# Kernel optimization log

Hardware: AMD Instinct MI355X
Metric: run time of the kernel (lower is better)

The kernel has to match this reference:

```python
import jax, jax.numpy as jnp
import numpy as np

DIM, NH, NKV = 1024, 16, 4
HD = DIM // NH  # 64
B, T = 2, 2048


def _rotary_freqs(seq_len, dim):
    inv_freq = 1.0 / (10000.0 ** (jnp.arange(0, dim, 2, dtype=jnp.float32) / dim))
    pos = jnp.arange(seq_len, dtype=jnp.float32)
    return pos[:, None] * inv_freq[None, :]  # [T, dim/2]


def _apply_rotary(x, freqs):
    # x: [B, H, T, HD]; freqs: [T, HD/2]
    x1, x2 = x[..., ::2], x[..., 1::2]
    cos, sin = jnp.cos(freqs), jnp.sin(freqs)
    # NOTE: faithful to source, second half is x1*sin - x2*cos (not +)
    return jnp.concatenate([x1 * cos - x2 * sin, x1 * sin - x2 * cos], axis=-1)


def setup_inputs() -> dict:
    key = jax.random.key(0)
    ks = jax.random.split(key, 5)
    s = 0.02
    return {
        "x": jax.random.normal(ks[0], (B, T, DIM), dtype=jnp.float32),
        "Wq": jax.random.normal(ks[1], (DIM, DIM), dtype=jnp.float32) * s,
        "bq": jnp.zeros((DIM,), jnp.float32),
        "Wk": jax.random.normal(ks[2], (DIM, NKV * HD), dtype=jnp.float32) * s,
        "bk": jnp.zeros((NKV * HD,), jnp.float32),
        "Wv": jax.random.normal(ks[3], (DIM, NKV * HD), dtype=jnp.float32) * s,
        "bv": jnp.zeros((NKV * HD,), jnp.float32),
        "Wo": jax.random.normal(ks[4], (DIM, DIM), dtype=jnp.float32) * s,
        "bo": jnp.zeros((DIM,), jnp.float32),
    }


def reference(x, Wq, bq, Wk, bk, Wv, bv, Wo, bo):
    Bx, Tx, C = x.shape
    q = (x @ Wq + bq).reshape(Bx, Tx, NH, HD).transpose(0, 2, 1, 3)   # [B,NH,T,HD]
    k = (x @ Wk + bk).reshape(Bx, Tx, NKV, HD).transpose(0, 2, 1, 3)  # [B,NKV,T,HD]
    v = (x @ Wv + bv).reshape(Bx, Tx, NKV, HD).transpose(0, 2, 1, 3)

    freqs = _rotary_freqs(Tx, HD)
    q = _apply_rotary(q, freqs)
    k = _apply_rotary(k, freqs)

    rep = NH // NKV
    k = jnp.repeat(k, rep, axis=1)  # [B,NH,T,HD]
    v = jnpp = jnp.repeat(v, rep, axis=1)

    scores = jnp.einsum('bhqd,bhkd->bhqk', q, k) / jnp.sqrt(jnp.float32(HD))
    causal = jnp.tril(jnp.ones((Tx, Tx), dtype=bool))
    scores = jnp.where(causal[None, None], scores, -jnp.inf)
    attn = jax.nn.softmax(scores, axis=-1)
    ctx = jnp.einsum('bhqk,bhkd->bhqd', attn, v)
    out = ctx.transpose(0, 2, 1, 3).reshape(Bx, Tx, C)
    return out @ Wo + bo
```

## Files before the change

### kernel.cpp

```cpp
#include <hip/hip_runtime.h>
#include <math.h>

#define DIM 1024
#define NH 16
#define NKV 4
#define HD 64
#define HALF 32
#define NB 2
#define SEQ 2048
#define KVD 256
#define MTOT 4096
#define QSCALE 0.18033688f
#define MBIAS 8.0f

typedef __bf16 bf16x8 __attribute__((ext_vector_type(8)));
typedef float f32x4 __attribute__((ext_vector_type(4)));
typedef unsigned short u16x8 __attribute__((ext_vector_type(8)));

#define MFMA16(a, b, c) __builtin_amdgcn_mfma_f32_16x16x32_bf16(a, b, c, 0, 0, 0)

__device__ __forceinline__ unsigned short f2bf(float f) {
    unsigned int u = __float_as_uint(f);
    u = (u + 0x7fffu + ((u >> 16) & 1u)) >> 16;
    return (unsigned short)u;
}

__device__ __forceinline__ unsigned cvt_pk(float lo, float hi) {
    unsigned r;
    asm("v_cvt_pk_bf16_f32 %0, %1, %2" : "=v"(r) : "v"(lo), "v"(hi));
    return r;
}

__device__ __forceinline__ void gll16(const unsigned short* g, unsigned short* l) {
    __builtin_amdgcn_global_load_lds((const __attribute__((address_space(1))) void*)g,
                                     (__attribute__((address_space(3))) void*)l, 16, 0, 0);
}

__global__ __launch_bounds__(256) void prep_kernel(
    const float* __restrict__ x,
    const float* __restrict__ Wq, const float* __restrict__ Wk,
    const float* __restrict__ Wv, const float* __restrict__ Wo,
    unsigned short* __restrict__ xb,
    unsigned short* __restrict__ qt, unsigned short* __restrict__ kt,
    unsigned short* __restrict__ vt, unsigned short* __restrict__ ot,
    float* __restrict__ cosb, float* __restrict__ sinb)
{
    __shared__ float tile[64][65];
    const int bx = blockIdx.x;
    const int tid = threadIdx.x;
    if (bx < 256) {
        int idx = bx * 256 + tid;
        int t = idx >> 5, d = idx & 31;
        float e = (float)(2 * d) / (float)HD;
        float invf = 1.0f / powf(10000.0f, e);
        float f = (float)t * invf;
        cosb[idx] = cosf(f);
        sinb[idx] = sinf(f);
    } else if (bx < 2304) {
        int i = ((bx - 256) * 256 + tid) * 8;
        float4 v0 = *(const float4*)&x[i];
        float4 v1 = *(const float4*)&x[i + 4];
        u16x8 o;
        o[0] = f2bf(v0.x); o[1] = f2bf(v0.y); o[2] = f2bf(v0.z); o[3] = f2bf(v0.w);
        o[4] = f2bf(v1.x); o[5] = f2bf(v1.y); o[6] = f2bf(v1.z); o[7] = f2bf(v1.w);
        *(u16x8*)&xb[i] = o;
    } else {
        int idx2 = bx - 2304;
        int z = idx2 >> 8, rem = idx2 & 255, xx = rem & 15, yy = rem >> 4;
        const float* W; unsigned short* Wt; int N;
        switch (z) {
            case 0: W = Wq; Wt = qt; N = DIM; break;
            case 1: W = Wk; Wt = kt; N = KVD; break;
            case 2: W = Wv; Wt = vt; N = KVD; break;
            default: W = Wo; Wt = ot; N = DIM; break;
        }
        const int n0 = xx * 64;
        if (n0 >= N) return;
        const int k0 = yy * 64;
        const int row = tid >> 2, coff = (tid & 3) * 16;
#pragma unroll
        for (int i = 0; i < 4; i++) {
            float4 v = *(const float4*)&W[(size_t)(k0 + row) * N + n0 + coff + i * 4];
            tile[row][coff + i * 4 + 0] = v.x; tile[row][coff + i * 4 + 1] = v.y;
            tile[row][coff + i * 4 + 2] = v.z; tile[row][coff + i * 4 + 3] = v.w;
        }
        __syncthreads();
        u16x8 a, b;
#pragma unroll
        for (int i = 0; i < 8; i++) a[i] = f2bf(tile[coff + i][row]);
#pragma unroll
        for (int i = 0; i < 8; i++) b[i] = f2bf(tile[coff + 8 + i][row]);
        *(u16x8*)&Wt[(size_t)(n0 + row) * DIM + k0 + coff] = a;
        *(u16x8*)&Wt[(size_t)(n0 + row) * DIM + k0 + coff + 8] = b;
    }
}

__global__ __launch_bounds__(256) void qkv_gemm_kernel(
    const unsigned short* __restrict__ xb,
    const unsigned short* __restrict__ wqt, const unsigned short* __restrict__ wkt,
    const unsigned short* __restrict__ wvt,
    const float* __restrict__ bq, const float* __restrict__ bk, const float* __restrict__ bv,
    const float* __restrict__ cosb, const float* __restrict__ sinb,
    unsigned short* __restrict__ qbuf, unsigned short* __restrict__ kbuf,
    unsigned short* __restrict__ vT)
{
    __shared__ unsigned short As[128 * 32];
    __shared__ unsigned short Bs[128 * 32];
    const int tid = threadIdx.x;
    const int lane = tid & 63, w = tid >> 6;
    const int l15 = lane & 15, lg = lane >> 4;
    const int bid = blockIdx.x;
    const int lid = (bid & 7) * 48 + (bid >> 3);
    const int m0 = (lid / 12) * 128;
    const int n0g = (lid % 12) * 128;

    const unsigned short* Wt; const float* bias; int n0, mode;
    if (n0g < DIM)            { Wt = wqt; bias = bq; n0 = n0g; mode = 0; }
    else if (n0g < DIM + KVD) { Wt = wkt; bias = bk; n0 = n0g - DIM; mode = 1; }
    else                      { Wt = wvt; bias = bv; n0 = n0g - DIM - KVD; mode = 2; }

    const int wr = w >> 1, wc = w & 1;

    f32x4 acc[4][4];
#pragma unroll
    for (int i = 0; i < 4; i++)
#pragma unroll
        for (int j = 0; j < 4; j++) acc[i][j] = (f32x4){0.f, 0.f, 0.f, 0.f};

    for (int k0 = 0; k0 < DIM; k0 += 32) {
        __syncthreads();
#pragma unroll
        for (int i = 0; i < 2; i++) {
            int S = i * 256 + w * 64 + lane;
            int r = S >> 2, c8 = (S & 3) * 8;
            gll16(xb + (size_t)(m0 + r) * DIM + k0 + c8, &As[(i * 256 + w * 64) * 8]);
            gll16(Wt + (size_t)(n0 + r) * DIM + k0 + c8, &Bs[(i * 256 + w * 64) * 8]);
        }
        __syncthreads();
        bf16x8 af[4], bfr[4];
#pragma unroll
        for (int r = 0; r < 4; r++)
            af[r] = *(const bf16x8*)&As[(wr * 64 + r * 16 + l15) * 32 + lg * 8];
#pragma unroll
        for (int c = 0; c < 4; c++)
            bfr[c] = *(const bf16x8*)&Bs[(wc * 64 + c * 16 + l15) * 32 + lg * 8];
#pragma unroll
        for (int r = 0; r < 4; r++)
#pragma unroll
            for (int c = 0; c < 4; c++)
                acc[r][c] = MFMA16(af[r], bfr[c], acc[r][c]);
    }

    const int nloc = n0 + wc * 64;
    const bool even = (l15 & 1) == 0;
#pragma unroll
    for (int rt = 0; rt < 4; rt++) {
#pragma unroll
        for (int ct = 0; ct < 4; ct++) {
            const int c = ct * 16 + l15;
            const float bsv = bias[nloc + c];
            if (mode == 2) {
                const int col = nloc + c;
                const int khh = col >> 6, d = col & 63;
                const int bb = m0 >> 11;
                const int t = (m0 & (SEQ - 1)) + wr * 64 + rt * 16 + lg * 4;
                float v0 = acc[rt][ct][0] + bsv;
                float v1 = acc[rt][ct][1] + bsv;
                float v2 = acc[rt][ct][2] + bsv;
                float v3 = acc[rt][ct][3] + bsv;
                unsigned short* dst = vT + ((size_t)(bb * NKV + khh) * 64 + d) * SEQ + t;
                *(uint2*)dst = make_uint2(cvt_pk(v0, v1), cvt_pk(v2, v3));
            } else {
                const int p = c >> 1;
#pragma unroll
                for (int q = 0; q < 4; q++) {
                    const int mrow = m0 + wr * 64 + rt * 16 + lg * 4 + q;
                    float val = acc[rt][ct][q] + bsv;
                    float prt = __shfl_xor(val, 1);
                    const int t = mrow & (SEQ - 1);
                    float cs = cosb[t * HALF + p];
                    float sn = sinb[t * HALF + p];
                    float outv = even ? (val * cs - prt * sn) : (prt * sn - val * cs);
                    int outc = even ? p : (p + 32);
                    if (mode == 0) qbuf[(size_t)mrow * DIM + nloc + outc] = f2bf(outv * QSCALE);
                    else           kbuf[(size_t)mrow * KVD + nloc + outc] = f2bf(outv);
                }
            }
        }
    }
}

__global__ __launch_bounds__(256, 4) void attn_mfma_kernel(
    const unsigned short* __restrict__ qb, const unsigned short* __restrict__ kb,
    const unsigned short* __restrict__ vT, unsigned short* __restrict__ ctx)
{
    __shared__ unsigned short Ks[2][64 * 64];
    __shared__ unsigned short Vt[2][64 * 64];
    __shared__ unsigned Pw[4][16 * 32];

    const int tid = threadIdx.x;
    const int lane = tid & 63, w = tid >> 6;
    const int l15 = lane & 15, lg = lane >> 4;
    const int h = blockIdx.y;
    const int b = blockIdx.z;
    const int kh = h >> 2;
    const int g = h + NH * b;
    const int tile = (blockIdx.x + g) & 31;
    const int q0 = tile * 64;

    const unsigned short* kg = kb + (size_t)b * SEQ * KVD + (size_t)kh * HD;
    const unsigned short* vg = vT + ((size_t)(b * NKV + kh) * HD) * SEQ;

    const int qg_row = w * 16 + l15;
    const int swzd = (l15 & 7) << 3;
    unsigned* PW = &Pw[w][l15 * 32];
    const int pswz = (l15 & 7) << 2;

    const unsigned short* qptr = qb + ((size_t)(b * SEQ + q0 + qg_row) * DIM + h * HD + lg * 8);
    bf16x8 bq0 = *(const bf16x8*)qptr;
    bf16x8 bq1 = *(const bf16x8*)(qptr + 32);

    const int S1 = w * 64 + lane, r1 = S1 >> 3, d81 = ((S1 & 7) ^ (r1 & 7)) * 8;
    const int S2 = 256 + w * 64 + lane, r2 = S2 >> 3, d82 = ((S2 & 7) ^ (r2 & 7)) * 8;

    gll16(kg + (size_t)r1 * KVD + d81, &Ks[0][(w * 64) * 8]);
    gll16(vg + (size_t)r1 * SEQ + d81, &Vt[0][(w * 64) * 8]);
    gll16(kg + (size_t)r2 * KVD + d82, &Ks[0][(256 + w * 64) * 8]);
    gll16(vg + (size_t)r2 * SEQ + d82, &Vt[0][(256 + w * 64) * 8]);
    __syncthreads();

    f32x4 o[4];
#pragma unroll
    for (int i = 0; i < 4; i++) o[i] = (f32x4){0.f, 0.f, 0.f, 0.f};
    float lrun = 0.f;

    const int nch = tile + 1;
#pragma unroll 1
    for (int ch = 0; ch < nch; ch++) {
        const int cur = ch & 1;
        if (ch + 1 < nch) {
            const int kv1 = (ch + 1) * 64;
            gll16(kg + (size_t)(kv1 + r1) * KVD + d81, &Ks[cur ^ 1][(w * 64) * 8]);
            gll16(vg + (size_t)r1 * SEQ + kv1 + d81,   &Vt[cur ^ 1][(w * 64) * 8]);
            gll16(kg + (size_t)(kv1 + r2) * KVD + d82, &Ks[cur ^ 1][(256 + w * 64) * 8]);
            gll16(vg + (size_t)r2 * SEQ + kv1 + d82,   &Vt[cur ^ 1][(256 + w * 64) * 8]);
        }

        f32x4 sacc[4];
#pragma unroll
        for (int i = 0; i < 4; i++) sacc[i] = (f32x4){0.f, 0.f, 0.f, 0.f};
        __builtin_amdgcn_s_setprio(1);
#pragma unroll
        for (int ct = 0; ct < 4; ct++) {
            const int kr = ct * 16 + l15;
            bf16x8 ak = *(const bf16x8*)&Ks[cur][kr * 64 + ((lg * 8) ^ swzd)];
            sacc[ct] = MFMA16(ak, bq0, sacc[ct]);
        }
#pragma unroll
        for (int ct = 0; ct < 4; ct++) {
            const int kr = ct * 16 + l15;
            bf16x8 ak = *(const bf16x8*)&Ks[cur][kr * 64 + ((32 + lg * 8) ^ swzd)];
            sacc[ct] = MFMA16(ak, bq1, sacc[ct]);
        }
        __builtin_amdgcn_s_setprio(0);

        if (ch == nch - 1) {
#pragma unroll
            for (int ct = 0; ct < 4; ct++)
#pragma unroll
                for (int r = 0; r < 4; r++)
                    if (ct * 16 + lg * 4 + r > qg_row) sacc[ct][r] = -INFINITY;
        }

        float rs = 0.f;
        unsigned pk0[4], pk1[4];
#pragma unroll
        for (int ct = 0; ct < 4; ct++) {
            float p0 = exp2f(sacc[ct][0] - MBIAS);
            float p1 = exp2f(sacc[ct][1] - MBIAS);
            float p2 = exp2f(sacc[ct][2] - MBIAS);
            float p3 = exp2f(sacc[ct][3] - MBIAS);
            rs += (p0 + p1) + (p2 + p3);
            pk0[ct] = cvt_pk(p0, p1);
            pk1[ct] = cvt_pk(p2, p3);
        }
        lrun += rs;

#pragma unroll
        for (int ct = 0; ct < 4; ct++) {
            int wrd = (ct * 8 + lg * 2) ^ pswz;
            *(uint2*)&PW[wrd] = make_uint2(pk0[ct], pk1[ct]);
        }

        __builtin_amdgcn_s_setprio(1);
#pragma unroll
        for (int s = 0; s < 2; s++) {
            int wrd = (s * 16 + lg * 4) ^ pswz;
            bf16x8 ap = *(const bf16x8*)&PW[wrd];
#pragma unroll
            for (int dt = 0; dt < 4; dt++) {
                const int d = dt * 16 + l15;
                bf16x8 bv2 = *(const bf16x8*)&Vt[cur][d * 64 + ((s * 32 + lg * 8) ^ ((d & 7) << 3))];
                o[dt] = MFMA16(ap, bv2, o[dt]);
            }
        }
        __builtin_amdgcn_s_setprio(0);

        __syncthreads();
    }

    lrun += __shfl_xor(lrun, 16);
    lrun += __shfl_xor(lrun, 32);
    float linv = 1.0f / lrun;
    float lb0 = __shfl(linv, lg * 4 + 0);
    float lb1 = __shfl(linv, lg * 4 + 1);
    float lb2 = __shfl(linv, lg * 4 + 2);
    float lb3 = __shfl(linv, lg * 4 + 3);
#pragma unroll
    for (int dt = 0; dt < 4; dt++) {
        const size_t base = (size_t)(b * SEQ + q0 + w * 16 + lg * 4) * DIM + h * HD + dt * 16 + l15;
        ctx[base]           = f2bf(o[dt][0] * lb0);
        ctx[base + DIM]     = f2bf(o[dt][1] * lb1);
        ctx[base + 2 * DIM] = f2bf(o[dt][2] * lb2);
        ctx[base + 3 * DIM] = f2bf(o[dt][3] * lb3);
    }
}

__global__ __launch_bounds__(256) void outproj_kernel(
    const unsigned short* __restrict__ ctx, const unsigned short* __restrict__ wot,
    const float* __restrict__ bo, float* __restrict__ out)
{
    __shared__ unsigned short As[128 * 32];
    __shared__ unsigned short Bs[128 * 32];
    const int tid = threadIdx.x;
    const int lane = tid & 63, w = tid >> 6;
    const int l15 = lane & 15, lg = lane >> 4;
    const int bid = blockIdx.x;
    const int lid = (bid & 7) * 32 + (bid >> 3);
    const int m0 = (lid >> 3) * 128;
    const int n0 = (lid & 7) * 128;
    const int wr = w >> 1, wc = w & 1;

    f32x4 acc[4][4];
#pragma unroll
    for (int i = 0; i < 4; i++)
#pragma unroll
        for (int j = 0; j < 4; j++) acc[i][j] = (f32x4){0.f, 0.f, 0.f, 0.f};

    for (int k0 = 0; k0 < DIM; k0 += 32) {
        __syncthreads();
#pragma unroll
        for (int i = 0; i < 2; i++) {
            int S = i * 256 + w * 64 + lane;
            int r = S >> 2, c8 = (S & 3) * 8;
            gll16(ctx + (size_t)(m0 + r) * DIM + k0 + c8, &As[(i * 256 + w * 64) * 8]);
            gll16(wot + (size_t)(n0 + r) * DIM + k0 + c8, &Bs[(i * 256 + w * 64) * 8]);
        }
        __syncthreads();
        bf16x8 af[4], bfr[4];
#pragma unroll
        for (int r = 0; r < 4; r++)
            af[r] = *(const bf16x8*)&As[(wr * 64 + r * 16 + l15) * 32 + lg * 8];
#pragma unroll
        for (int c = 0; c < 4; c++)
            bfr[c] = *(const bf16x8*)&Bs[(wc * 64 + c * 16 + l15) * 32 + lg * 8];
#pragma unroll
        for (int r = 0; r < 4; r++)
#pragma unroll
            for (int c = 0; c < 4; c++)
                acc[r][c] = MFMA16(af[r], bfr[c], acc[r][c]);
    }

#pragma unroll
    for (int rt = 0; rt < 4; rt++) {
#pragma unroll
        for (int ct = 0; ct < 4; ct++) {
            const int ncol = n0 + wc * 64 + ct * 16 + l15;
            const float bsv = bo[ncol];
#pragma unroll
            for (int q = 0; q < 4; q++) {
                const int mrow = m0 + wr * 64 + rt * 16 + lg * 4 + q;
                out[(size_t)mrow * DIM + ncol] = acc[rt][ct][q] + bsv;
            }
        }
    }
}

extern "C" void kernel_launch(void* const* d_in, const int* in_sizes, int n_in,
                              void* d_out, int out_size, void* d_ws, size_t ws_size,
                              hipStream_t stream) {
    (void)in_sizes; (void)n_in; (void)out_size; (void)ws_size;
    const float* x  = (const float*)d_in[0];
    const float* Wq = (const float*)d_in[1];
    const float* bq = (const float*)d_in[2];
    const float* Wk = (const float*)d_in[3];
    const float* bk = (const float*)d_in[4];
    const float* Wv = (const float*)d_in[5];
    const float* bv = (const float*)d_in[6];
    const float* Wo = (const float*)d_in[7];
    const float* bo = (const float*)d_in[8];
    float* out = (float*)d_out;
    char* ws = (char*)d_ws;

    unsigned short* xb  = (unsigned short*)(ws);
    unsigned short* qbf = (unsigned short*)(ws + 8388608);
    unsigned short* kbf = (unsigned short*)(ws + 16777216);
    unsigned short* ctx = (unsigned short*)(ws + 20971520);
    unsigned short* wqt = (unsigned short*)(ws + 29360128);
    unsigned short* wkt = (unsigned short*)(ws + 31457280);
    unsigned short* wvt = (unsigned short*)(ws + 31981568);
    unsigned short* wot = (unsigned short*)(ws + 32505856);
    float* cosb = (float*)(ws + 34603008);
    float* sinb = (float*)(ws + 34865152);
    unsigned short* vTb = (unsigned short*)(ws + 35127296);

    hipLaunchKernelGGL(prep_kernel, dim3(3328), dim3(256), 0, stream,
                       x, Wq, Wk, Wv, Wo, xb, wqt, wkt, wvt, wot, cosb, sinb);
    hipLaunchKernelGGL(qkv_gemm_kernel, dim3(384), dim3(256), 0, stream,
                       xb, wqt, wkt, wvt, bq, bk, bv, cosb, sinb, qbf, kbf, vTb);
    hipLaunchKernelGGL(attn_mfma_kernel, dim3(32, NH, NB), dim3(256), 0, stream,
                       qbf, kbf, vTb, ctx);
    hipLaunchKernelGGL(outproj_kernel, dim3(256), dim3(256), 0, stream,
                       ctx, wot, bo, out);
}
```

Baseline: 111.0 us.

## Halve GEMM M-tiles and make attention waves process two query sub-tiles

The QKV and output-projection GEMMs now use 64x128 tiles instead of 128x128, doubling the grid (768 and 512 blocks) to fill more compute units on a small problem. The attention kernel drops to 2 waves per block, and each wave handles 32 query rows as two 16-row sub-tiles that share every K and V fragment read from LDS. This halves LDS fragment traffic per MFMA and raises ILP, but also halves threads per block for staging and raises register pressure. The launch bounds change to (128, 2).

```diff
diff --git a/kernel.cpp b/kernel.cpp
--- a/kernel.cpp
+++ b/kernel.cpp
@@ -104,14 +104,14 @@
     unsigned short* __restrict__ qbuf, unsigned short* __restrict__ kbuf,
     unsigned short* __restrict__ vT)
 {
-    __shared__ unsigned short As[128 * 32];
+    __shared__ unsigned short As[64 * 32];
     __shared__ unsigned short Bs[128 * 32];
     const int tid = threadIdx.x;
     const int lane = tid & 63, w = tid >> 6;
     const int l15 = lane & 15, lg = lane >> 4;
     const int bid = blockIdx.x;
-    const int lid = (bid & 7) * 48 + (bid >> 3);
-    const int m0 = (lid / 12) * 128;
+    const int lid = (bid & 7) * 96 + (bid >> 3);
+    const int m0 = (lid / 12) * 64;
     const int n0g = (lid % 12) * 128;
 
     const unsigned short* Wt; const float* bias; int n0, mode;
@@ -120,32 +120,33 @@
     else                      { Wt = wvt; bias = bv; n0 = n0g - DIM - KVD; mode = 2; }
 
     const int wr = w >> 1, wc = w & 1;
-
-    f32x4 acc[4][4];
-#pragma unroll
-    for (int i = 0; i < 4; i++)
+    const int Ar = tid >> 2, Ac8 = (tid & 3) * 8;
+
+    f32x4 acc[2][4];
+#pragma unroll
+    for (int i = 0; i < 2; i++)
 #pragma unroll
         for (int j = 0; j < 4; j++) acc[i][j] = (f32x4){0.f, 0.f, 0.f, 0.f};
 
     for (int k0 = 0; k0 < DIM; k0 += 32) {
         __syncthreads();
+        gll16(xb + (size_t)(m0 + Ar) * DIM + k0 + Ac8, &As[(tid & ~63) * 8]);
 #pragma unroll
         for (int i = 0; i < 2; i++) {
-            int S = i * 256 + w * 64 + lane;
+            int S = i * 256 + tid;
             int r = S >> 2, c8 = (S & 3) * 8;
-            gll16(xb + (size_t)(m0 + r) * DIM + k0 + c8, &As[(i * 256 + w * 64) * 8]);
-            gll16(Wt + (size_t)(n0 + r) * DIM + k0 + c8, &Bs[(i * 256 + w * 64) * 8]);
-        }
-        __syncthreads();
-        bf16x8 af[4], bfr[4];
-#pragma unroll
-        for (int r = 0; r < 4; r++)
-            af[r] = *(const bf16x8*)&As[(wr * 64 + r * 16 + l15) * 32 + lg * 8];
+            gll16(Wt + (size_t)(n0 + r) * DIM + k0 + c8, &Bs[(i * 256 + (tid & ~63)) * 8]);
+        }
+        __syncthreads();
+        bf16x8 af[2], bfr[4];
+#pragma unroll
+        for (int r = 0; r < 2; r++)
+            af[r] = *(const bf16x8*)&As[(wr * 32 + r * 16 + l15) * 32 + lg * 8];
 #pragma unroll
         for (int c = 0; c < 4; c++)
             bfr[c] = *(const bf16x8*)&Bs[(wc * 64 + c * 16 + l15) * 32 + lg * 8];
 #pragma unroll
-        for (int r = 0; r < 4; r++)
+        for (int r = 0; r < 2; r++)
 #pragma unroll
             for (int c = 0; c < 4; c++)
                 acc[r][c] = MFMA16(af[r], bfr[c], acc[r][c]);
@@ -154,7 +155,7 @@
     const int nloc = n0 + wc * 64;
     const bool even = (l15 & 1) == 0;
 #pragma unroll
-    for (int rt = 0; rt < 4; rt++) {
+    for (int rt = 0; rt < 2; rt++) {
 #pragma unroll
         for (int ct = 0; ct < 4; ct++) {
             const int c = ct * 16 + l15;
@@ -163,7 +164,7 @@
                 const int col = nloc + c;
                 const int khh = col >> 6, d = col & 63;
                 const int bb = m0 >> 11;
-                const int t = (m0 & (SEQ - 1)) + wr * 64 + rt * 16 + lg * 4;
+                const int t = (m0 & (SEQ - 1)) + wr * 32 + rt * 16 + lg * 4;
                 float v0 = acc[rt][ct][0] + bsv;
                 float v1 = acc[rt][ct][1] + bsv;
                 float v2 = acc[rt][ct][2] + bsv;
@@ -174,7 +175,7 @@
                 const int p = c >> 1;
 #pragma unroll
                 for (int q = 0; q < 4; q++) {
-                    const int mrow = m0 + wr * 64 + rt * 16 + lg * 4 + q;
+                    const int mrow = m0 + wr * 32 + rt * 16 + lg * 4 + q;
                     float val = acc[rt][ct][q] + bsv;
                     float prt = __shfl_xor(val, 1);
                     const int t = mrow & (SEQ - 1);
@@ -190,13 +191,13 @@
     }
 }
 
-__global__ __launch_bounds__(256, 4) void attn_mfma_kernel(
+__global__ __launch_bounds__(128, 2) void attn_mfma_kernel(
     const unsigned short* __restrict__ qb, const unsigned short* __restrict__ kb,
     const unsigned short* __restrict__ vT, unsigned short* __restrict__ ctx)
 {
     __shared__ unsigned short Ks[2][64 * 64];
     __shared__ unsigned short Vt[2][64 * 64];
-    __shared__ unsigned Pw[4][16 * 32];
+    __shared__ unsigned Pw[2][2][16 * 32];
 
     const int tid = threadIdx.x;
     const int lane = tid & 63, w = tid >> 6;
@@ -211,28 +212,39 @@
     const unsigned short* kg = kb + (size_t)b * SEQ * KVD + (size_t)kh * HD;
     const unsigned short* vg = vT + ((size_t)(b * NKV + kh) * HD) * SEQ;
 
-    const int qg_row = w * 16 + l15;
     const int swzd = (l15 & 7) << 3;
-    unsigned* PW = &Pw[w][l15 * 32];
     const int pswz = (l15 & 7) << 2;
-
-    const unsigned short* qptr = qb + ((size_t)(b * SEQ + q0 + qg_row) * DIM + h * HD + lg * 8);
-    bf16x8 bq0 = *(const bf16x8*)qptr;
-    bf16x8 bq1 = *(const bf16x8*)(qptr + 32);
-
-    const int S1 = w * 64 + lane, r1 = S1 >> 3, d81 = ((S1 & 7) ^ (r1 & 7)) * 8;
-    const int S2 = 256 + w * 64 + lane, r2 = S2 >> 3, d82 = ((S2 & 7) ^ (r2 & 7)) * 8;
-
-    gll16(kg + (size_t)r1 * KVD + d81, &Ks[0][(w * 64) * 8]);
-    gll16(vg + (size_t)r1 * SEQ + d81, &Vt[0][(w * 64) * 8]);
-    gll16(kg + (size_t)r2 * KVD + d82, &Ks[0][(256 + w * 64) * 8]);
-    gll16(vg + (size_t)r2 * SEQ + d82, &Vt[0][(256 + w * 64) * 8]);
+    unsigned* PW0 = &Pw[w][0][l15 * 32];
+    unsigned* PW1 = &Pw[w][1][l15 * 32];
+
+    bf16x8 bq[2][2];
+#pragma unroll
+    for (int s2 = 0; s2 < 2; s2++) {
+        const unsigned short* qptr = qb +
+            ((size_t)(b * SEQ + q0 + w * 32 + s2 * 16 + l15) * DIM + h * HD + lg * 8);
+        bq[s2][0] = *(const bf16x8*)qptr;
+        bq[s2][1] = *(const bf16x8*)(qptr + 32);
+    }
+
+#define STAGE(bufK, bufV, kvoff)                                                   \
+    _Pragma("unroll")                                                              \
+    for (int i = 0; i < 4; i++) {                                                  \
+        int S = i * 128 + tid;                                                     \
+        int r = S >> 3, qd = S & 7;                                                \
+        int d8 = ((qd ^ (r & 7))) * 8;                                             \
+        gll16(kg + (size_t)((kvoff) + r) * KVD + d8, &(bufK)[(i * 128 + (tid & ~63)) * 8]); \
+        gll16(vg + (size_t)r * SEQ + (kvoff) + d8,   &(bufV)[(i * 128 + (tid & ~63)) * 8]); \
+    }
+
+    STAGE(Ks[0], Vt[0], 0)
     __syncthreads();
 
-    f32x4 o[4];
-#pragma unroll
-    for (int i = 0; i < 4; i++) o[i] = (f32x4){0.f, 0.f, 0.f, 0.f};
-    float lrun = 0.f;
+    f32x4 o[2][4];
+#pragma unroll
+    for (int s2 = 0; s2 < 2; s2++)
+#pragma unroll
+        for (int i = 0; i < 4; i++) o[s2][i] = (f32x4){0.f, 0.f, 0.f, 0.f};
+    float lrun0 = 0.f, lrun1 = 0.f;
 
     const int nch = tile + 1;
 #pragma unroll 1
@@ -240,68 +252,68 @@
         const int cur = ch & 1;
         if (ch + 1 < nch) {
             const int kv1 = (ch + 1) * 64;
-            gll16(kg + (size_t)(kv1 + r1) * KVD + d81, &Ks[cur ^ 1][(w * 64) * 8]);
-            gll16(vg + (size_t)r1 * SEQ + kv1 + d81,   &Vt[cur ^ 1][(w * 64) * 8]);
-            gll16(kg + (size_t)(kv1 + r2) * KVD + d82, &Ks[cur ^ 1][(256 + w * 64) * 8]);
-            gll16(vg + (size_t)r2 * SEQ + kv1 + d82,   &Vt[cur ^ 1][(256 + w * 64) * 8]);
-        }
-
-        f32x4 sacc[4];
-#pragma unroll
-        for (int i = 0; i < 4; i++) sacc[i] = (f32x4){0.f, 0.f, 0.f, 0.f};
+            STAGE(Ks[cur ^ 1], Vt[cur ^ 1], kv1)
+        }
+
+        f32x4 sacc[2][4];
+#pragma unroll
+        for (int s2 = 0; s2 < 2; s2++)
+#pragma unroll
+            for (int i = 0; i < 4; i++) sacc[s2][i] = (f32x4){0.f, 0.f, 0.f, 0.f};
         __builtin_amdgcn_s_setprio(1);
 #pragma unroll
+        for (int s = 0; s < 2; s++) {
+#pragma unroll
+            for (int ct = 0; ct < 4; ct++) {
+                const int kr = ct * 16 + l15;
+                bf16x8 ak = *(const bf16x8*)&Ks[cur][kr * 64 + ((s * 32 + lg * 8) ^ swzd)];
+                sacc[0][ct] = MFMA16(ak, bq[0][s], sacc[0][ct]);
+                sacc[1][ct] = MFMA16(ak, bq[1][s], sacc[1][ct]);
+            }
+        }
+        __builtin_amdgcn_s_setprio(0);
+
+        if (ch == nch - 1) {
+#pragma unroll
+            for (int s2 = 0; s2 < 2; s2++) {
+                const int ql = w * 32 + s2 * 16 + l15;
+#pragma unroll
+                for (int ct = 0; ct < 4; ct++)
+#pragma unroll
+                    for (int r = 0; r < 4; r++)
+                        if (ct * 16 + lg * 4 + r > ql) sacc[s2][ct][r] = -INFINITY;
+            }
+        }
+
+#pragma unroll
         for (int ct = 0; ct < 4; ct++) {
-            const int kr = ct * 16 + l15;
-            bf16x8 ak = *(const bf16x8*)&Ks[cur][kr * 64 + ((lg * 8) ^ swzd)];
-            sacc[ct] = MFMA16(ak, bq0, sacc[ct]);
-        }
-#pragma unroll
-        for (int ct = 0; ct < 4; ct++) {
-            const int kr = ct * 16 + l15;
-            bf16x8 ak = *(const bf16x8*)&Ks[cur][kr * 64 + ((32 + lg * 8) ^ swzd)];
-            sacc[ct] = MFMA16(ak, bq1, sacc[ct]);
-        }
-        __builtin_amdgcn_s_setprio(0);
-
-        if (ch == nch - 1) {
-#pragma unroll
-            for (int ct = 0; ct < 4; ct++)
-#pragma unroll
-                for (int r = 0; r < 4; r++)
-                    if (ct * 16 + lg * 4 + r > qg_row) sacc[ct][r] = -INFINITY;
-        }
-
-        float rs = 0.f;
-        unsigned pk0[4], pk1[4];
-#pragma unroll
-        for (int ct = 0; ct < 4; ct++) {
-            float p0 = exp2f(sacc[ct][0] - MBIAS);
-            float p1 = exp2f(sacc[ct][1] - MBIAS);
-            float p2 = exp2f(sacc[ct][2] - MBIAS);
-            float p3 = exp2f(sacc[ct][3] - MBIAS);
-            rs += (p0 + p1) + (p2 + p3);
-            pk0[ct] = cvt_pk(p0, p1);
-            pk1[ct] = cvt_pk(p2, p3);
-        }
-        lrun += rs;
-
-#pragma unroll
-        for (int ct = 0; ct < 4; ct++) {
+            float a0 = exp2f(sacc[0][ct][0] - MBIAS);
+            float a1 = exp2f(sacc[0][ct][1] - MBIAS);
+            float a2 = exp2f(sacc[0][ct][2] - MBIAS);
+            float a3 = exp2f(sacc[0][ct][3] - MBIAS);
+            lrun0 += (a0 + a1) + (a2 + a3);
             int wrd = (ct * 8 + lg * 2) ^ pswz;
-            *(uint2*)&PW[wrd] = make_uint2(pk0[ct], pk1[ct]);
+            *(uint2*)&PW0[wrd] = make_uint2(cvt_pk(a0, a1), cvt_pk(a2, a3));
+            float b0 = exp2f(sacc[1][ct][0] - MBIAS);
+            float b1 = exp2f(sacc[1][ct][1] - MBIAS);
+            float b2 = exp2f(sacc[1][ct][2] - MBIAS);
+            float b3 = exp2f(sacc[1][ct][3] - MBIAS);
+            lrun1 += (b0 + b1) + (b2 + b3);
+            *(uint2*)&PW1[wrd] = make_uint2(cvt_pk(b0, b1), cvt_pk(b2, b3));
         }
 
         __builtin_amdgcn_s_setprio(1);
 #pragma unroll
         for (int s = 0; s < 2; s++) {
             int wrd = (s * 16 + lg * 4) ^ pswz;
-            bf16x8 ap = *(const bf16x8*)&PW[wrd];
+            bf16x8 ap0 = *(const bf16x8*)&PW0[wrd];
+            bf16x8 ap1 = *(const bf16x8*)&PW1[wrd];
 #pragma unroll
             for (int dt = 0; dt < 4; dt++) {
                 const int d = dt * 16 + l15;
                 bf16x8 bv2 = *(const bf16x8*)&Vt[cur][d * 64 + ((s * 32 + lg * 8) ^ ((d & 7) << 3))];
-                o[dt] = MFMA16(ap, bv2, o[dt]);
+                o[0][dt] = MFMA16(ap0, bv2, o[0][dt]);
+                o[1][dt] = MFMA16(ap1, bv2, o[1][dt]);
             }
         }
         __builtin_amdgcn_s_setprio(0);
@@ -309,20 +321,27 @@
         __syncthreads();
     }
 
-    lrun += __shfl_xor(lrun, 16);
-    lrun += __shfl_xor(lrun, 32);
-    float linv = 1.0f / lrun;
-    float lb0 = __shfl(linv, lg * 4 + 0);
-    float lb1 = __shfl(linv, lg * 4 + 1);
-    float lb2 = __shfl(linv, lg * 4 + 2);
-    float lb3 = __shfl(linv, lg * 4 + 3);
-#pragma unroll
-    for (int dt = 0; dt < 4; dt++) {
-        const size_t base = (size_t)(b * SEQ + q0 + w * 16 + lg * 4) * DIM + h * HD + dt * 16 + l15;
-        ctx[base]           = f2bf(o[dt][0] * lb0);
-        ctx[base + DIM]     = f2bf(o[dt][1] * lb1);
-        ctx[base + 2 * DIM] = f2bf(o[dt][2] * lb2);
-        ctx[base + 3 * DIM] = f2bf(o[dt][3] * lb3);
+    lrun0 += __shfl_xor(lrun0, 16);
+    lrun0 += __shfl_xor(lrun0, 32);
+    lrun1 += __shfl_xor(lrun1, 16);
+    lrun1 += __shfl_xor(lrun1, 32);
+    float li0 = 1.0f / lrun0, li1 = 1.0f / lrun1;
+#pragma unroll
+    for (int s2 = 0; s2 < 2; s2++) {
+        float li = (s2 == 0) ? li0 : li1;
+        float lb0 = __shfl(li, lg * 4 + 0);
+        float lb1 = __shfl(li, lg * 4 + 1);
+        float lb2 = __shfl(li, lg * 4 + 2);
+        float lb3 = __shfl(li, lg * 4 + 3);
+#pragma unroll
+        for (int dt = 0; dt < 4; dt++) {
+            const size_t base = (size_t)(b * SEQ + q0 + w * 32 + s2 * 16 + lg * 4) * DIM
+                                + h * HD + dt * 16 + l15;
+            ctx[base]           = f2bf(o[s2][dt][0] * lb0);
+            ctx[base + DIM]     = f2bf(o[s2][dt][1] * lb1);
+            ctx[base + 2 * DIM] = f2bf(o[s2][dt][2] * lb2);
+            ctx[base + 3 * DIM] = f2bf(o[s2][dt][3] * lb3);
+        }
     }
 }
 
@@ -330,56 +349,57 @@
     const unsigned short* __restrict__ ctx, const unsigned short* __restrict__ wot,
     const float* __restrict__ bo, float* __restrict__ out)
 {
-    __shared__ unsigned short As[128 * 32];
+    __shared__ unsigned short As[64 * 32];
     __shared__ unsigned short Bs[128 * 32];
     const int tid = threadIdx.x;
     const int lane = tid & 63, w = tid >> 6;
     const int l15 = lane & 15, lg = lane >> 4;
     const int bid = blockIdx.x;
-    const int lid = (bid & 7) * 32 + (bid >> 3);
-    const int m0 = (lid >> 3) * 128;
+    const int lid = (bid & 7) * 64 + (bid >> 3);
+    const int m0 = (lid >> 3) * 64;
     const int n0 = (lid & 7) * 128;
     const int wr = w >> 1, wc = w & 1;
-
-    f32x4 acc[4][4];
-#pragma unroll
-    for (int i = 0; i < 4; i++)
+    const int Ar = tid >> 2, Ac8 = (tid & 3) * 8;
+
+    f32x4 acc[2][4];
+#pragma unroll
+    for (int i = 0; i < 2; i++)
 #pragma unroll
         for (int j = 0; j < 4; j++) acc[i][j] = (f32x4){0.f, 0.f, 0.f, 0.f};
 
     for (int k0 = 0; k0 < DIM; k0 += 32) {
         __syncthreads();
+        gll16(ctx + (size_t)(m0 + Ar) * DIM + k0 + Ac8, &As[(tid & ~63) * 8]);
 #pragma unroll
         for (int i = 0; i < 2; i++) {
-            int S = i * 256 + w * 64 + lane;
+            int S = i * 256 + tid;
             int r = S >> 2, c8 = (S & 3) * 8;
-            gll16(ctx + (size_t)(m0 + r) * DIM + k0 + c8, &As[(i * 256 + w * 64) * 8]);
-            gll16(wot + (size_t)(n0 + r) * DIM + k0 + c8, &Bs[(i * 256 + w * 64) * 8]);
-        }
-        __syncthreads();
-        bf16x8 af[4], bfr[4];
-#pragma unroll
-        for (int r = 0; r < 4; r++)
-            af[r] = *(const bf16x8*)&As[(wr * 64 + r * 16 + l15) * 32 + lg * 8];
+            gll16(wot + (size_t)(n0 + r) * DIM + k0 + c8, &Bs[(i * 256 + (tid & ~63)) * 8]);
+        }
+        __syncthreads();
+        bf16x8 af[2], bfr[4];
+#pragma unroll
+        for (int r = 0; r < 2; r++)
+            af[r] = *(const bf16x8*)&As[(wr * 32 + r * 16 + l15) * 32 + lg * 8];
 #pragma unroll
         for (int c = 0; c < 4; c++)
             bfr[c] = *(const bf16x8*)&Bs[(wc * 64 + c * 16 + l15) * 32 + lg * 8];
 #pragma unroll
-        for (int r = 0; r < 4; r++)
+        for (int r = 0; r < 2; r++)
 #pragma unroll
             for (int c = 0; c < 4; c++)
                 acc[r][c] = MFMA16(af[r], bfr[c], acc[r][c]);
     }
 
 #pragma unroll
-    for (int rt = 0; rt < 4; rt++) {
+    for (int rt = 0; rt < 2; rt++) {
 #pragma unroll
         for (int ct = 0; ct < 4; ct++) {
             const int ncol = n0 + wc * 64 + ct * 16 + l15;
             const float bsv = bo[ncol];
 #pragma unroll
             for (int q = 0; q < 4; q++) {
-                const int mrow = m0 + wr * 64 + rt * 16 + lg * 4 + q;
+                const int mrow = m0 + wr * 32 + rt * 16 + lg * 4 + q;
                 out[(size_t)mrow * DIM + ncol] = acc[rt][ct][q] + bsv;
             }
         }
@@ -416,10 +436,10 @@
 
     hipLaunchKernelGGL(prep_kernel, dim3(3328), dim3(256), 0, stream,
                        x, Wq, Wk, Wv, Wo, xb, wqt, wkt, wvt, wot, cosb, sinb);
-    hipLaunchKernelGGL(qkv_gemm_kernel, dim3(384), dim3(256), 0, stream,
+    hipLaunchKernelGGL(qkv_gemm_kernel, dim3(768), dim3(256), 0, stream,
                        xb, wqt, wkt, wvt, bq, bk, bv, cosb, sinb, qbf, kbf, vTb);
-    hipLaunchKernelGGL(attn_mfma_kernel, dim3(32, NH, NB), dim3(256), 0, stream,
+    hipLaunchKernelGGL(attn_mfma_kernel, dim3(32, NH, NB), dim3(128), 0, stream,
                        qbf, kbf, vTb, ctx);
-    hipLaunchKernelGGL(outproj_kernel, dim3(256), dim3(256), 0, stream,
+    hipLaunchKernelGGL(outproj_kernel, dim3(512), dim3(256), 0, stream,
                        ctx, wot, bo, out);
 }
```

After: 116.8 us. 1.05x slower.
